# Optimization experiments

Measured on AMD Instinct MI355X. Metric: run time of the kernel, lower is better.

Reference implementation:

```python
import jax, jax.numpy as jnp
import numpy as np

# SDNet-CTRL cfg constants
MU = 0.1          # FISTA step size (cfg['MODEL']['MU'])
LMBD = 0.1        # sparsity weight (cfg['MODEL']['LAMBDA'][0])
N_STEPS = 4       # FISTA iterations (cfg['MODEL']['NUM_LAYERS'])
EPS_BN = 1e-5


def _conv(x, w, stride, padding):
    # torch F.conv2d, NCHW / OIHW
    return jax.lax.conv_general_dilated(
        x, w, window_strides=(stride, stride),
        padding=[(padding, padding), (padding, padding)],
        dimension_numbers=('NCHW', 'OIHW', 'NCHW'))


def _conv_t(c, w, stride, padding):
    # torch F.conv_transpose2d(c, w, stride, padding) with output_padding chosen
    # so that it exactly inverts the spatial map of _conv (k=4,s=2,p=1 -> 0).
    k = w.shape[2]
    w_t = jnp.flip(w, (2, 3)).transpose(1, 0, 2, 3)  # (I,O,k,k) flipped
    pad = k - 1 - padding
    return jax.lax.conv_general_dilated(
        c, w_t, window_strides=(1, 1),
        padding=[(pad, pad), (pad, pad)],
        lhs_dilation=(stride, stride),
        dimension_numbers=('NCHW', 'OIHW', 'NCHW'))


def _shrink_nn(c, thr):
    # non-negative soft threshold (cfg NONEGATIVE=True)
    return jax.nn.relu(c - thr)


def _dict_conv(x, w, stride, padding):
    # DictBlock: FISTA convolutional sparse coding, n_dict=1, w_norm=True.
    # normalize each dictionary atom (output filter) to unit l2 norm
    wn = w * jax.lax.rsqrt(jnp.sum(w * w, axis=(1, 2, 3), keepdims=True))
    ss = MU
    thr = LMBD * ss
    # t = 0
    c = _shrink_nn(ss * _conv(x, wn, stride, padding), thr)
    c_pre_pre = jnp.zeros_like(c)
    c_pre = c
    tk = 1.0
    for t in range(1, N_STEPS):
        tk_pre = tk
        tk = (1.0 + float(np.sqrt(1.0 + 4.0 * tk_pre * tk_pre))) / 2.0
        y = c_pre + ((tk_pre - 1.0) / tk) * (c_pre - c_pre_pre)
        r = x - _conv_t(y, wn, stride, padding)      # residual in image space
        c = _shrink_nn(y + ss * _conv(r, wn, stride, padding), thr)
        c_pre_pre, c_pre = c_pre, c
    return c


def _bn(x, g, b):
    # training-mode BatchNorm2d (batch statistics)
    m = jnp.mean(x, axis=(0, 2, 3), keepdims=True)
    v = jnp.var(x, axis=(0, 2, 3), keepdims=True)
    return g.reshape(1, -1, 1, 1) * (x - m) * jax.lax.rsqrt(v + EPS_BN) + b.reshape(1, -1, 1, 1)


def _lrelu(x):
    return jnp.where(x >= 0, x, 0.2 * x)


def setup_inputs() -> dict:
    key = jax.random.key(0)
    ks = jax.random.split(key, 5)
    nc, ndf, nz = 3, 128, 256
    B, H = 256, 32

    def mk_w(k, o, i):
        return jax.random.normal(k, (o, i, 4, 4), jnp.float32) * 0.02

    return {
        'x': jax.random.normal(ks[0], (B, nc, H, H), jnp.float32),
        'w1': mk_w(ks[1], ndf, nc),
        'w2': mk_w(ks[2], 2 * ndf, ndf),
        'w3': mk_w(ks[3], 4 * ndf, 2 * ndf),
        'w4': mk_w(ks[4], nz, 4 * ndf),
        'g2': jnp.ones((2 * ndf,), jnp.float32),
        'b2': jnp.zeros((2 * ndf,), jnp.float32),
        'g3': jnp.ones((4 * ndf,), jnp.float32),
        'b3': jnp.zeros((4 * ndf,), jnp.float32),
    }


def reference(x, w1, w2, w3, w4, g2, b2, g3, b3):
    h = _lrelu(_dict_conv(x, w1, 2, 1))                 # (B, ndf, 16, 16)
    h = _lrelu(_bn(_dict_conv(h, w2, 2, 1), g2, b2))    # (B, 2ndf, 8, 8)
    h = _lrelu(_bn(_dict_conv(h, w3, 2, 1), g3, b3))    # (B, 4ndf, 4, 4)
    h = _dict_conv(h, w4, 1, 0)                         # (B, nz, 1, 1)
    h = h.reshape(h.shape[0], -1)                       # Flatten
    n = jnp.sqrt(jnp.sum(h * h, axis=1, keepdims=True))
    return h / jnp.maximum(n, 1e-12)                    # F.normalize(dim=1)
```

## Files before the change

### kernel.cpp

```cpp
#include <hip/hip_runtime.h>
#include <math.h>

#define SS   0.1f
#define THRC 0.01f

typedef __attribute__((ext_vector_type(8))) short s16x8;
typedef __attribute__((ext_vector_type(4))) float f32x4;

__device__ __forceinline__ float b2f(unsigned short u){
  union{unsigned int i; float f;} v; v.i = ((unsigned int)u)<<16; return v.f;
}
__device__ __forceinline__ unsigned short f2b(float f){
  union{float f; unsigned int i;} v; v.f = f;
  return (unsigned short)((v.i + 0x7fffu + ((v.i>>16)&1u))>>16);
}
__device__ __forceinline__ s16x8 as_s16x8(uint4 u){
  union{uint4 a; s16x8 b;} c; c.a = u; return c.b;
}
__device__ __forceinline__ int swz8(int row, int q){ return (row<<3) | (q ^ (row&7)); }

__device__ __forceinline__ void gld16(const void* g, void* l){
  __builtin_amdgcn_global_load_lds(
      (const __attribute__((address_space(1))) unsigned int*)g,
      (__attribute__((address_space(3))) unsigned int*)l, 16, 0, 0);
}

enum { EPI_FIRST=0, EPI_UPDATE=1, EPI_PARTIAL=2, EPI_RES_NHWC=3, EPI_RES_FLAT=4 };

struct EpiM {
  unsigned short* C;
  const unsigned short* Y;
  const unsigned short* Cprev;
  unsigned short* Yout;
  const unsigned short* img;
  const unsigned short* zp;
  float coef;
  int lH, lW, lC;
  int S_MN, Kc;
};

struct LA_ident {
  const unsigned short* A; int K;
  __device__ void setz(int){}
  __device__ __forceinline__ const unsigned short* addr(int m, int k8) const {
    return A + (size_t)m*K + ((size_t)k8<<3);
  }
};
struct LA_nhwc {
  const unsigned short* img; const unsigned short* zp; int lH, lW, lC;
  __device__ void setz(int){}
  __device__ __forceinline__ const unsigned short* addr(int m, int k8) const {
    int lWo = lW-1, lHo = lH-1;
    int wo = m & ((1<<lWo)-1); int t = m>>lWo; int ho = t & ((1<<lHo)-1); int b = t>>lHo;
    int k = k8<<3; int kk = k>>lC; int i = k & ((1<<lC)-1);
    int kw = kk&3, kh = kk>>2;
    int h = 2*ho + kh - 1, w = 2*wo + kw - 1;
    if ((unsigned)h >= (1u<<lH) || (unsigned)w >= (1u<<lW)) return zp;
    return img + (((((((size_t)b<<lH)|h)<<lW)|w))<<lC) + i;
  }
};
struct LA_yg {
  const unsigned short* y; const unsigned short* zp; int lHo, lWo, lO, ph, pw;
  __device__ void setz(int z){ ph = z>>1; pw = z&1; }
  __device__ __forceinline__ const unsigned short* addr(int m, int k8) const {
    int l = m & ((1<<lWo)-1); int t = m>>lWo; int j = t & ((1<<lHo)-1); int b = t>>lHo;
    int k = k8<<3; int tt = k>>lO; int o = k & ((1<<lO)-1);
    int th = tt>>1, tw = tt&1;
    int ho = ph ? (j+1-th) : (j-th);
    int wo = pw ? (l+1-tw) : (l-tw);
    if ((unsigned)ho >= (1u<<lHo) || (unsigned)wo >= (1u<<lWo)) return zp;
    return y + (((((((size_t)b<<lHo)|ho)<<lWo)|wo))<<lO) + o;
  }
};
struct LA_padb {
  const unsigned short* img;
  __device__ void setz(int){}
  __device__ __forceinline__ const unsigned short* addr(int m, int k8) const {
    int wo = m&15, t = m>>4, ho = t&15, b = t>>4;
    int kh = k8>>1, kw0 = (k8&1)<<1;
    int h = 2*ho + kh, w = 2*wo + kw0;
    return img + (((size_t)b*34 + h)*34 + w)*4;
  }
};

template<class AL, int EPI>
__global__ __launch_bounds__(512)
void mgemm_k(AL al, const unsigned short* __restrict__ Bw, int M, int N, int K, EpiM ep)
{
  __shared__ uint4 S[2][2048];
  const int tid = threadIdx.x;
  const int bm = blockIdx.y<<7, bn = blockIdx.x<<7;
  const int z = blockIdx.z;
  int kb = 0, ke = K;
  const unsigned short* Bp = Bw;
  if (EPI == EPI_PARTIAL){ kb = z*ep.Kc; ke = kb + ep.Kc; }
  if (EPI == EPI_RES_NHWC){ Bp = Bw + (size_t)z*(size_t)N*K; al.setz(z); }

  f32x4 acc[4][2];
  #pragma unroll
  for (int i=0;i<4;++i)
    #pragma unroll
    for (int j=0;j<2;++j){ acc[i][j][0]=0.f; acc[i][j][1]=0.f; acc[i][j][2]=0.f; acc[i][j][3]=0.f; }

  const int lane = tid & 63, wid = tid >> 6;
  const int wm = (wid>>2)<<6, wn = (wid&3)<<5;
  const int fr = lane & 15, fq = lane >> 4;

  auto issue = [&](int k0, int b){
    int k8 = k0>>3;
    #pragma unroll
    for (int i=0;i<2;++i){
      int s  = (wid<<7) + (i<<6) + lane;
      int sr = s>>3, q = (s&7) ^ (sr&7);
      gld16(al.addr(bm+sr, k8+q), (void*)&S[b][(wid<<7) + (i<<6)]);
    }
    #pragma unroll
    for (int i=0;i<2;++i){
      int s  = (wid<<7) + (i<<6) + lane;
      int sr = s>>3, q = (s&7) ^ (sr&7);
      int gn = bn + sr;
      const unsigned short* src = (gn < N) ? Bp + (size_t)gn*K + ((size_t)(k8+q)<<3) : ep.zp;
      gld16(src, (void*)&S[b][1024 + (wid<<7) + (i<<6)]);
    }
  };

  issue(kb, 0);
  int buf = 0;
  for (int k0 = kb; k0 < ke; k0 += 64){
    asm volatile("s_waitcnt vmcnt(0)" ::: "memory");
    __builtin_amdgcn_s_barrier();
    __builtin_amdgcn_sched_barrier(0);
    if (k0 + 64 < ke) issue(k0 + 64, buf^1);
    const uint4* As = &S[buf][0];
    const uint4* Bs = &S[buf][1024];
    #pragma unroll
    for (int half=0; half<2; ++half){
      const int qb = (half<<2) | fq;
      s16x8 af[4], bf[2];
      #pragma unroll
      for (int mi=0;mi<4;++mi) af[mi] = as_s16x8(As[swz8(wm + mi*16 + fr, qb)]);
      #pragma unroll
      for (int ni=0;ni<2;++ni) bf[ni] = as_s16x8(Bs[swz8(wn + ni*16 + fr, qb)]);
      #pragma unroll
      for (int mi=0;mi<4;++mi)
        #pragma unroll
        for (int ni=0;ni<2;++ni)
          acc[mi][ni] = __builtin_amdgcn_mfma_f32_16x16x32_bf16(af[mi], bf[ni], acc[mi][ni], 0,0,0);
    }
    buf ^= 1;
  }

  #pragma unroll
  for (int mi=0;mi<4;++mi){
    #pragma unroll
    for (int ni=0;ni<2;++ni){
      int n = bn + wn + ni*16 + fr;
      if (n >= N) continue;
      int mb = bm + wm + mi*16 + (fq<<2);
      #pragma unroll
      for (int r=0;r<4;++r){
        int m = mb + r;
        float a = acc[mi][ni][r];
        if (EPI == EPI_FIRST){
          float v = SS*a - THRC; v = v>0.f ? v : 0.f;
          ep.C[(size_t)m*N + n] = f2b(v);
        } else if (EPI == EPI_UPDATE){
          size_t idx = (size_t)m*N + n;
          float v = b2f(ep.Y[idx]) + SS*a - THRC; v = v>0.f ? v : 0.f;
          ep.C[idx] = f2b(v);
          if (ep.Yout) ep.Yout[idx] = f2b(v + ep.coef*(v - b2f(ep.Cprev[idx])));
        } else if (EPI == EPI_PARTIAL){
          ep.C[(size_t)z*ep.S_MN + (size_t)m*N + n] = f2b(a);
        } else if (EPI == EPI_RES_NHWC){
          int lWo = ep.lW-1, lHo = ep.lH-1;
          int l = m & ((1<<lWo)-1); int t = m>>lWo; int j = t & ((1<<lHo)-1); int b = t>>lHo;
          int h = 2*j + (z>>1), w = 2*l + (z&1);
          size_t ridx = (((((((size_t)b<<ep.lH)|h)<<ep.lW)|w))<<ep.lC) | n;
          ep.C[ridx] = f2b(b2f(ep.img[ridx]) - a);
        } else {
          size_t ridx = (size_t)m*N + n;
          ep.C[ridx] = f2b(b2f(ep.img[ridx]) - a);
        }
      }
    }
  }
}

__global__ __launch_bounds__(64)
void wnorm1_k(const float* __restrict__ w, unsigned short* __restrict__ wf1,
              unsigned short* __restrict__ wcolT)
{
  int o = blockIdx.x, tid = threadIdx.x;
  __shared__ float red[64];
  float v = (tid < 48) ? w[(size_t)o*48 + tid] : 0.f;
  red[tid] = v*v; __syncthreads();
  for (int d=32; d>0; d>>=1){ if (tid<d) red[tid] += red[tid+d]; __syncthreads(); }
  float nv = v * rsqrtf(red[0]);
  if (tid < 48){
    int c = tid>>4, t = tid&15;
    wf1[(size_t)o*64 + t*4 + c] = f2b(nv);
    wcolT[(size_t)(t*4+c)*128 + o] = f2b(nv);
  } else {
    int t = tid - 48;
    wf1[(size_t)o*64 + t*4 + 3] = 0;
    wcolT[(size_t)(t*4+3)*128 + o] = 0;
  }
}
__global__ __launch_bounds__(256)
void wnormX_k(const float* __restrict__ w, int Cin, int O,
              unsigned short* __restrict__ wT, unsigned short* __restrict__ wclsT,
              unsigned short* __restrict__ wEO)
{
  int o = blockIdx.x, tid = threadIdx.x; int E = Cin*16;
  __shared__ float red[256];
  float s = 0.f;
  for (int e = tid; e < E; e += 256){ float v = w[(size_t)o*E + e]; s += v*v; }
  red[tid] = s; __syncthreads();
  for (int d=128; d>0; d>>=1){ if (tid<d) red[tid] += red[tid+d]; __syncthreads(); }
  float scale = rsqrtf(red[0]);
  for (int e = tid; e < E; e += 256){
    float v = w[(size_t)o*E + e] * scale;
    int i = e>>4, t = e&15, kh = t>>2, kw = t&3;
    int ee = t*Cin + i;
    if (wT)  wT[(size_t)o*E + ee] = f2b(v);
    if (wEO) wEO[(size_t)ee*O + o] = f2b(v);
    if (wclsT){
      int ph = (kh&1)^1, pw = (kw&1)^1, cls = ph*2+pw;
      int tt = (kh>>1)*2 + (kw>>1);
      wclsT[(((size_t)cls*Cin + i)*4 + tt)*O + o] = f2b(v);
    }
  }
}

__global__ void splitk_shrink_k(const unsigned short* __restrict__ part,
                                const unsigned short* __restrict__ Y,
                                unsigned short* __restrict__ C,
                                unsigned short* __restrict__ Yout,
                                const unsigned short* __restrict__ Cprev,
                                float coef, int MN, int S)
{
  for (int i = blockIdx.x*blockDim.x + threadIdx.x; i < MN; i += gridDim.x*blockDim.x){
    float s = 0.f;
    for (int zz = 0; zz < S; ++zz) s += b2f(part[(size_t)zz*MN + i]);
    float v = (Y ? b2f(Y[i]) : 0.f) + SS*s - THRC; v = v>0.f ? v : 0.f;
    C[i] = f2b(v);
    if (Yout) Yout[i] = f2b(v + coef*(v - b2f(Cprev[i])));
  }
}

__global__ void pad_x_k(const float* __restrict__ x, unsigned short* __restrict__ xpb){
  int idx = blockIdx.x*256 + threadIdx.x;
  if (idx >= 262144) return;
  int w = idx&31, t = idx>>5, h = t&31, b = t>>5;
  size_t src = (size_t)b*3072 + h*32 + w;
  unsigned short* d = xpb + (((size_t)b*34 + h+1)*34 + w+1)*4;
  d[0] = f2b(x[src]); d[1] = f2b(x[src+1024]); d[2] = f2b(x[src+2048]); d[3] = 0;
}

__global__ void l1_resid_k(const unsigned short* __restrict__ Col,
                           const float* __restrict__ x, unsigned short* __restrict__ r1pb)
{
  int idx = blockIdx.x*256 + threadIdx.x;
  if (idx >= 262144) return;
  int w = idx&31, t = idx>>5, h = t&31, b = t>>5;
  float a0=0.f, a1=0.f, a2=0.f;
  #pragma unroll
  for (int kh=0; kh<4; ++kh){
    int hh = h+1-kh; if (hh & 1) continue; int ho = hh>>1; if ((unsigned)ho >= 16u) continue;
    #pragma unroll
    for (int kw=0; kw<4; ++kw){
      int ww = w+1-kw; if (ww & 1) continue; int wo = ww>>1; if ((unsigned)wo >= 16u) continue;
      int m = (b*16+ho)*16+wo;
      const unsigned short* cp = Col + (size_t)m*64 + (kh*4+kw)*4;
      a0 += b2f(cp[0]); a1 += b2f(cp[1]); a2 += b2f(cp[2]);
    }
  }
  size_t src = (size_t)b*3072 + h*32 + w;
  unsigned short* d = r1pb + (((size_t)b*34 + h+1)*34 + w+1)*4;
  d[0] = f2b(x[src] - a0); d[1] = f2b(x[src+1024] - a1); d[2] = f2b(x[src+2048] - a2); d[3] = 0;
}

__global__ void bn_stats_k(const unsigned short* __restrict__ d, float* __restrict__ sums,
                           int rows, int O){
  for (int c = threadIdx.x; c < O; c += blockDim.x){
    float a = 0.f, b = 0.f;
    for (int r = blockIdx.x; r < rows; r += gridDim.x){
      float v = b2f(d[(size_t)r*O + c]); a += v; b += v*v;
    }
    atomicAdd(&sums[c], a); atomicAdd(&sums[O+c], b);
  }
}
__global__ void bn_apply_k(const unsigned short* __restrict__ d, const float* __restrict__ sums,
                           const float* __restrict__ g, const float* __restrict__ bta,
                           unsigned short* __restrict__ outp, int rows, int O, float inv_cnt){
  int total = rows*O;
  for (int i = blockIdx.x*blockDim.x + threadIdx.x; i < total; i += gridDim.x*blockDim.x){
    int c = i % O;
    float mean = sums[c]*inv_cnt;
    float var  = sums[O+c]*inv_cnt - mean*mean;
    float v = g[c]*(b2f(d[i])-mean)*rsqrtf(var + 1e-5f) + bta[c];
    outp[i] = f2b(v >= 0.f ? v : 0.2f*v);
  }
}

__global__ __launch_bounds__(256)
void norm_rows_k(const unsigned short* __restrict__ h, float* __restrict__ out){
  int row = blockIdx.x, tid = threadIdx.x;
  __shared__ float red[256];
  float v = b2f(h[(size_t)row*256 + tid]);
  red[tid] = v*v; __syncthreads();
  for (int d=128; d>0; d>>=1){ if (tid<d) red[tid] += red[tid+d]; __syncthreads(); }
  float nrm = sqrtf(red[0]); nrm = nrm > 1e-12f ? nrm : 1e-12f;
  out[(size_t)row*256 + tid] = v / nrm;
}

extern "C" void kernel_launch(void* const* d_in, const int* in_sizes, int n_in,
                              void* d_out, int out_size, void* d_ws, size_t ws_size,
                              hipStream_t stream)
{
  const float* x  = (const float*)d_in[0];
  const float* w1 = (const float*)d_in[1];
  const float* w2 = (const float*)d_in[2];
  const float* w3 = (const float*)d_in[3];
  const float* w4 = (const float*)d_in[4];
  const float* g2 = (const float*)d_in[5];
  const float* b2 = (const float*)d_in[6];
  const float* g3 = (const float*)d_in[7];
  const float* b3 = (const float*)d_in[8];
  float* out = (float*)d_out;

  char* p = (char*)d_ws;
  auto ah = [&](size_t n){ unsigned short* r = (unsigned short*)p; p += n*2; return r; };
  auto af = [&](size_t n){ float* r = (float*)p; p += n*4; return r; };

  unsigned short* wf1    = ah(128*64);
  unsigned short* wcol1T = ah(64*128);
  unsigned short* wT2    = ah((size_t)256*2048);
  unsigned short* wcls2  = ah((size_t)4*128*1024);
  unsigned short* wT3    = ah((size_t)512*4096);
  unsigned short* wcls3  = ah((size_t)4*256*2048);
  unsigned short* wT4    = ah((size_t)256*8192);
  unsigned short* wE4    = ah((size_t)8192*256);
  unsigned short* h1     = ah((size_t)8388608);
  unsigned short* h2     = ah((size_t)4194304);
  unsigned short* h3     = ah((size_t)2097152);
  unsigned short* cA     = ah((size_t)8388608);
  unsigned short* cB     = ah((size_t)8388608);
  unsigned short* yA     = ah((size_t)8388608);
  unsigned short* yB     = ah((size_t)8388608);
  unsigned short* rH     = ah((size_t)8388608);
  char* regionA = p; p += 17858560;
  unsigned short* Col    = (unsigned short*)regionA;
  unsigned short* xpb    = (unsigned short*)(regionA + 8388608);
  unsigned short* r1pb   = (unsigned short*)(regionA + 8388608 + 2367488);
  unsigned short* partL3 = (unsigned short*)regionA;
  unsigned short* partL4 = (unsigned short*)regionA;
  float* bnsum = af(1024);
  unsigned short* zp16 = ah(128);

  double tk = 1.0; float coef[4] = {0.f,0.f,0.f,0.f};
  for (int t = 1; t < 4; ++t){
    double tkp = tk; tk = (1.0 + sqrt(1.0 + 4.0*tkp*tkp))*0.5;
    coef[t] = (float)((tkp - 1.0)/tk);
  }

  hipMemsetAsync(zp16, 0, 256, stream);
  hipMemsetAsync(xpb,  0, 2367488, stream);
  hipMemsetAsync(r1pb, 0, 2367488, stream);
  pad_x_k<<<1024,256,0,stream>>>(x, xpb);
  wnorm1_k<<<128, 64, 0, stream>>>(w1, wf1, wcol1T);
  wnormX_k<<<256,256,0,stream>>>(w2, 128, 256, wT2, wcls2, nullptr);
  wnormX_k<<<512,256,0,stream>>>(w3, 256, 512, wT3, wcls3, nullptr);
  wnormX_k<<<256,256,0,stream>>>(w4, 512, 256, wT4, nullptr, wE4);

  auto l1_fwd = [&](const unsigned short* src, const unsigned short* Y, const unsigned short* Cp,
                    unsigned short* Cout, unsigned short* Yout, float cf){
    LA_padb al{src};
    EpiM ep{}; ep.C=Cout; ep.Y=Y; ep.Cprev=Cp; ep.Yout=Yout; ep.coef=cf; ep.zp=zp16;
    dim3 g(1, 512, 1);
    if (Y) mgemm_k<LA_padb,EPI_UPDATE><<<g,512,0,stream>>>(al, wf1, 65536,128,64, ep);
    else   mgemm_k<LA_padb,EPI_FIRST ><<<g,512,0,stream>>>(al, wf1, 65536,128,64, ep);
  };
  auto l1_tconv = [&](const unsigned short* y){
    LA_ident al{y, 128};
    EpiM ep{}; ep.C=Col; ep.S_MN=0; ep.Kc=128; ep.zp=zp16;
    mgemm_k<LA_ident,EPI_PARTIAL><<<dim3(1,512,1),512,0,stream>>>(al, wcol1T, 65536,64,128, ep);
    l1_resid_k<<<1024,256,0,stream>>>(Col, x, r1pb);
  };
  l1_fwd(xpb,  nullptr, nullptr, cA, nullptr, 0.f);
  l1_tconv(cA);
  l1_fwd(r1pb, cA, cA, cB, yA, coef[2]);
  l1_tconv(yA);
  l1_fwd(r1pb, yA, cB, cA, yB, coef[3]);
  l1_tconv(yB);
  l1_fwd(r1pb, yB, nullptr, h1, nullptr, 0.f);

  auto l2_fwd = [&](const unsigned short* src, const unsigned short* Y, const unsigned short* Cp,
                    unsigned short* Cout, unsigned short* Yout, float cf){
    LA_nhwc al{src, zp16, 4,4,7};
    EpiM ep{}; ep.C=Cout; ep.Y=Y; ep.Cprev=Cp; ep.Yout=Yout; ep.coef=cf; ep.zp=zp16;
    dim3 g(2, 128, 1);
    if (Y) mgemm_k<LA_nhwc,EPI_UPDATE><<<g,512,0,stream>>>(al, wT2, 16384,256,2048, ep);
    else   mgemm_k<LA_nhwc,EPI_FIRST ><<<g,512,0,stream>>>(al, wT2, 16384,256,2048, ep);
  };
  auto l2_tconv = [&](const unsigned short* y){
    LA_yg al{y, zp16, 3,3,8, 0,0};
    EpiM ep{}; ep.C=rH; ep.img=h1; ep.lH=4; ep.lW=4; ep.lC=7; ep.zp=zp16;
    mgemm_k<LA_yg,EPI_RES_NHWC><<<dim3(1,128,4),512,0,stream>>>(al, wcls2, 16384,128,1024, ep);
  };
  l2_fwd(h1, nullptr, nullptr, cA, nullptr, 0.f);
  l2_tconv(cA);
  l2_fwd(rH, cA, cA, cB, yA, coef[2]);
  l2_tconv(yA);
  l2_fwd(rH, yA, cB, cA, yB, coef[3]);
  l2_tconv(yB);
  l2_fwd(rH, yB, nullptr, cB, nullptr, 0.f);
  hipMemsetAsync(bnsum, 0, 2*256*sizeof(float), stream);
  bn_stats_k<<<256,256,0,stream>>>(cB, bnsum, 16384, 256);
  bn_apply_k<<<2048,256,0,stream>>>(cB, bnsum, g2, b2, h2, 16384, 256, 1.f/16384.f);

  auto l3_fwd = [&](const unsigned short* src, const unsigned short* Y, const unsigned short* Cp,
                    unsigned short* Cout, unsigned short* Yout, float cf){
    LA_nhwc al{src, zp16, 3,3,8};
    EpiM ep{}; ep.C=partL3; ep.S_MN=4096*512; ep.Kc=1024; ep.zp=zp16;
    mgemm_k<LA_nhwc,EPI_PARTIAL><<<dim3(4,32,4),512,0,stream>>>(al, wT3, 4096,512,4096, ep);
    splitk_shrink_k<<<1024,256,0,stream>>>(partL3, Y, Cout, Yout, Cp, cf, 4096*512, 4);
  };
  auto l3_tconv = [&](const unsigned short* y){
    LA_yg al{y, zp16, 2,2,9, 0,0};
    EpiM ep{}; ep.C=rH; ep.img=h2; ep.lH=3; ep.lW=3; ep.lC=8; ep.zp=zp16;
    mgemm_k<LA_yg,EPI_RES_NHWC><<<dim3(2,32,4),512,0,stream>>>(al, wcls3, 4096,256,2048, ep);
  };
  l3_fwd(h2, nullptr, nullptr, cA, nullptr, 0.f);
  l3_tconv(cA);
  l3_fwd(rH, cA, cA, cB, yA, coef[2]);
  l3_tconv(yA);
  l3_fwd(rH, yA, cB, cA, yB, coef[3]);
  l3_tconv(yB);
  l3_fwd(rH, yB, nullptr, cB, nullptr, 0.f);
  hipMemsetAsync(bnsum, 0, 2*512*sizeof(float), stream);
  bn_stats_k<<<256,256,0,stream>>>(cB, bnsum, 4096, 512);
  bn_apply_k<<<2048,256,0,stream>>>(cB, bnsum, g3, b3, h3, 4096, 512, 1.f/4096.f);

  auto l4_fwd = [&](const unsigned short* Asrc, const unsigned short* Y, const unsigned short* Cp,
                    unsigned short* Cout, unsigned short* Yout, float cf){
    LA_ident al{Asrc, 8192};
    EpiM ep{}; ep.C=partL4; ep.S_MN=65536; ep.Kc=256; ep.zp=zp16;
    mgemm_k<LA_ident,EPI_PARTIAL><<<dim3(2,2,32),512,0,stream>>>(al, wT4, 256,256,8192, ep);
    splitk_shrink_k<<<256,256,0,stream>>>(partL4, Y, Cout, Yout, Cp, cf, 65536, 32);
  };
  auto l4_tconv = [&](const unsigned short* y){
    LA_ident al{y, 256};
    EpiM ep{}; ep.C=rH; ep.img=h3; ep.zp=zp16;
    mgemm_k<LA_ident,EPI_RES_FLAT><<<dim3(64,2,1),512,0,stream>>>(al, wE4, 256,8192,256, ep);
  };
  l4_fwd(h3, nullptr, nullptr, cA, nullptr, 0.f);
  l4_tconv(cA);
  l4_fwd(rH, cA, cA, cB, yA, coef[2]);
  l4_tconv(yA);
  l4_fwd(rH, yA, cB, cA, yB, coef[3]);
  l4_tconv(yB);
  l4_fwd(rH, yB, nullptr, cB, nullptr, 0.f);

  norm_rows_k<<<256,256,0,stream>>>(cB, out);
}
```

Before: 889.3 us.

## Load GEMM B operand straight into registers, using 256-thread blocks

The shared GEMM kernel now runs with 256 threads and four waves instead of eight. Each wave computes a 64x64 sub-tile with a 4x4 grid of accumulators. Only the A tile is staged through LDS; the B fragments are read directly from global memory into registers, which are double-buffered across a k-loop unrolled by two. This halves LDS use and the number of barriers per tile, and should allow two blocks per CU. The cost is more accumulator registers and B reads that are not shared between waves. Those reads are scattered 16-byte loads and lose the old zero-pointer bounds guard when N is smaller than the tile width.

```diff
diff --git a/kernel.cpp b/kernel.cpp
--- a/kernel.cpp
+++ b/kernel.cpp
@@ -84,10 +84,10 @@
 };
 
 template<class AL, int EPI>
-__global__ __launch_bounds__(512)
+__global__ __launch_bounds__(256, 2)
 void mgemm_k(AL al, const unsigned short* __restrict__ Bw, int M, int N, int K, EpiM ep)
 {
-  __shared__ uint4 S[2][2048];
+  __shared__ uint4 S[2][1024];
   const int tid = threadIdx.x;
   const int bm = blockIdx.y<<7, bn = blockIdx.x<<7;
   const int z = blockIdx.z;
@@ -96,64 +96,70 @@
   if (EPI == EPI_PARTIAL){ kb = z*ep.Kc; ke = kb + ep.Kc; }
   if (EPI == EPI_RES_NHWC){ Bp = Bw + (size_t)z*(size_t)N*K; al.setz(z); }
 
-  f32x4 acc[4][2];
+  f32x4 acc[4][4];
   #pragma unroll
   for (int i=0;i<4;++i)
     #pragma unroll
-    for (int j=0;j<2;++j){ acc[i][j][0]=0.f; acc[i][j][1]=0.f; acc[i][j][2]=0.f; acc[i][j][3]=0.f; }
+    for (int j=0;j<4;++j){ acc[i][j][0]=0.f; acc[i][j][1]=0.f; acc[i][j][2]=0.f; acc[i][j][3]=0.f; }
 
   const int lane = tid & 63, wid = tid >> 6;
-  const int wm = (wid>>2)<<6, wn = (wid&3)<<5;
+  const int wm = (wid>>1)<<6, wn = (wid&1)<<6;
   const int fr = lane & 15, fq = lane >> 4;
 
-  auto issue = [&](int k0, int b){
+  auto issueA = [&](int k0, int b){
     int k8 = k0>>3;
     #pragma unroll
-    for (int i=0;i<2;++i){
-      int s  = (wid<<7) + (i<<6) + lane;
+    for (int i=0;i<4;++i){
+      int s  = (wid<<8) + (i<<6) + lane;
       int sr = s>>3, q = (s&7) ^ (sr&7);
-      gld16(al.addr(bm+sr, k8+q), (void*)&S[b][(wid<<7) + (i<<6)]);
-    }
-    #pragma unroll
-    for (int i=0;i<2;++i){
-      int s  = (wid<<7) + (i<<6) + lane;
-      int sr = s>>3, q = (s&7) ^ (sr&7);
-      int gn = bn + sr;
-      const unsigned short* src = (gn < N) ? Bp + (size_t)gn*K + ((size_t)(k8+q)<<3) : ep.zp;
-      gld16(src, (void*)&S[b][1024 + (wid<<7) + (i<<6)]);
-    }
-  };
-
-  issue(kb, 0);
+      gld16(al.addr(bm+sr, k8+q), (void*)&S[b][(wid<<8) + (i<<6)]);
+    }
+  };
+  auto loadB = [&](int k0, int ni, int half)->uint4{
+    int n = bn + wn + ni*16 + fr;
+    return *(const uint4*)(Bp + (size_t)n*K + k0 + (((half<<2)|fq)<<3));
+  };
+
+  uint4 bA[8], bB[8];
+  issueA(kb, 0);
+  #pragma unroll
+  for (int ni=0;ni<4;++ni){ bA[ni*2+0]=loadB(kb,ni,0); bA[ni*2+1]=loadB(kb,ni,1); }
+
   int buf = 0;
-  for (int k0 = kb; k0 < ke; k0 += 64){
+  auto stepf = [&](int k0, uint4 (&cur)[8], uint4 (&nxt)[8]){
     asm volatile("s_waitcnt vmcnt(0)" ::: "memory");
     __builtin_amdgcn_s_barrier();
     __builtin_amdgcn_sched_barrier(0);
-    if (k0 + 64 < ke) issue(k0 + 64, buf^1);
+    if (k0 + 64 < ke){
+      issueA(k0 + 64, buf^1);
+      #pragma unroll
+      for (int ni=0;ni<4;++ni){ nxt[ni*2+0]=loadB(k0+64,ni,0); nxt[ni*2+1]=loadB(k0+64,ni,1); }
+    }
     const uint4* As = &S[buf][0];
-    const uint4* Bs = &S[buf][1024];
     #pragma unroll
     for (int half=0; half<2; ++half){
       const int qb = (half<<2) | fq;
-      s16x8 af[4], bf[2];
+      s16x8 af[4];
       #pragma unroll
       for (int mi=0;mi<4;++mi) af[mi] = as_s16x8(As[swz8(wm + mi*16 + fr, qb)]);
       #pragma unroll
-      for (int ni=0;ni<2;++ni) bf[ni] = as_s16x8(Bs[swz8(wn + ni*16 + fr, qb)]);
-      #pragma unroll
       for (int mi=0;mi<4;++mi)
         #pragma unroll
-        for (int ni=0;ni<2;++ni)
-          acc[mi][ni] = __builtin_amdgcn_mfma_f32_16x16x32_bf16(af[mi], bf[ni], acc[mi][ni], 0,0,0);
+        for (int ni=0;ni<4;++ni)
+          acc[mi][ni] = __builtin_amdgcn_mfma_f32_16x16x32_bf16(
+              af[mi], as_s16x8(cur[ni*2+half]), acc[mi][ni], 0,0,0);
     }
     buf ^= 1;
+  };
+  for (int k0 = kb; k0 < ke; k0 += 128){
+    stepf(k0, bA, bB);
+    if (k0 + 64 < ke) stepf(k0+64, bB, bA);
   }
 
   #pragma unroll
   for (int mi=0;mi<4;++mi){
     #pragma unroll
-    for (int ni=0;ni<2;++ni){
+    for (int ni=0;ni<4;++ni){
       int n = bn + wn + ni*16 + fr;
       if (n >= N) continue;
       int mb = bm + wm + mi*16 + (fq<<2);
@@ -378,13 +384,13 @@
     LA_padb al{src};
     EpiM ep{}; ep.C=Cout; ep.Y=Y; ep.Cprev=Cp; ep.Yout=Yout; ep.coef=cf; ep.zp=zp16;
     dim3 g(1, 512, 1);
-    if (Y) mgemm_k<LA_padb,EPI_UPDATE><<<g,512,0,stream>>>(al, wf1, 65536,128,64, ep);
-    else   mgemm_k<LA_padb,EPI_FIRST ><<<g,512,0,stream>>>(al, wf1, 65536,128,64, ep);
+    if (Y) mgemm_k<LA_padb,EPI_UPDATE><<<g,256,0,stream>>>(al, wf1, 65536,128,64, ep);
+    else   mgemm_k<LA_padb,EPI_FIRST ><<<g,256,0,stream>>>(al, wf1, 65536,128,64, ep);
   };
   auto l1_tconv = [&](const unsigned short* y){
     LA_ident al{y, 128};
     EpiM ep{}; ep.C=Col; ep.S_MN=0; ep.Kc=128; ep.zp=zp16;
-    mgemm_k<LA_ident,EPI_PARTIAL><<<dim3(1,512,1),512,0,stream>>>(al, wcol1T, 65536,64,128, ep);
+    mgemm_k<LA_ident,EPI_PARTIAL><<<dim3(1,512,1),256,0,stream>>>(al, wcol1T, 65536,64,128, ep);
     l1_resid_k<<<1024,256,0,stream>>>(Col, x, r1pb);
   };
   l1_fwd(xpb,  nullptr, nullptr, cA, nullptr, 0.f);
@@ -400,13 +406,13 @@
     LA_nhwc al{src, zp16, 4,4,7};
     EpiM ep{}; ep.C=Cout; ep.Y=Y; ep.Cprev=Cp; ep.Yout=Yout; ep.coef=cf; ep.zp=zp16;
     dim3 g(2, 128, 1);
-    if (Y) mgemm_k<LA_nhwc,EPI_UPDATE><<<g,512,0,stream>>>(al, wT2, 16384,256,2048, ep);
-    else   mgemm_k<LA_nhwc,EPI_FIRST ><<<g,512,0,stream>>>(al, wT2, 16384,256,2048, ep);
+    if (Y) mgemm_k<LA_nhwc,EPI_UPDATE><<<g,256,0,stream>>>(al, wT2, 16384,256,2048, ep);
+    else   mgemm_k<LA_nhwc,EPI_FIRST ><<<g,256,0,stream>>>(al, wT2, 16384,256,2048, ep);
   };
   auto l2_tconv = [&](const unsigned short* y){
     LA_yg al{y, zp16, 3,3,8, 0,0};
     EpiM ep{}; ep.C=rH; ep.img=h1; ep.lH=4; ep.lW=4; ep.lC=7; ep.zp=zp16;
-    mgemm_k<LA_yg,EPI_RES_NHWC><<<dim3(1,128,4),512,0,stream>>>(al, wcls2, 16384,128,1024, ep);
+    mgemm_k<LA_yg,EPI_RES_NHWC><<<dim3(1,128,4),256,0,stream>>>(al, wcls2, 16384,128,1024, ep);
   };
   l2_fwd(h1, nullptr, nullptr, cA, nullptr, 0.f);
   l2_tconv(cA);
@@ -423,13 +429,13 @@
                     unsigned short* Cout, unsigned short* Yout, float cf){
     LA_nhwc al{src, zp16, 3,3,8};
     EpiM ep{}; ep.C=partL3; ep.S_MN=4096*512; ep.Kc=1024; ep.zp=zp16;
-    mgemm_k<LA_nhwc,EPI_PARTIAL><<<dim3(4,32,4),512,0,stream>>>(al, wT3, 4096,512,4096, ep);
+    mgemm_k<LA_nhwc,EPI_PARTIAL><<<dim3(4,32,4),256,0,stream>>>(al, wT3, 4096,512,4096, ep);
     splitk_shrink_k<<<1024,256,0,stream>>>(partL3, Y, Cout, Yout, Cp, cf, 4096*512, 4);
   };
   auto l3_tconv = [&](const unsigned short* y){
     LA_yg al{y, zp16, 2,2,9, 0,0};
     EpiM ep{}; ep.C=rH; ep.img=h2; ep.lH=3; ep.lW=3; ep.lC=8; ep.zp=zp16;
-    mgemm_k<LA_yg,EPI_RES_NHWC><<<dim3(2,32,4),512,0,stream>>>(al, wcls3, 4096,256,2048, ep);
+    mgemm_k<LA_yg,EPI_RES_NHWC><<<dim3(2,32,4),256,0,stream>>>(al, wcls3, 4096,256,2048, ep);
   };
   l3_fwd(h2, nullptr, nullptr, cA, nullptr, 0.f);
   l3_tconv(cA);
@@ -446,13 +452,13 @@
                     unsigned short* Cout, unsigned short* Yout, float cf){
     LA_ident al{Asrc, 8192};
     EpiM ep{}; ep.C=partL4; ep.S_MN=65536; ep.Kc=256; ep.zp=zp16;
-    mgemm_k<LA_ident,EPI_PARTIAL><<<dim3(2,2,32),512,0,stream>>>(al, wT4, 256,256,8192, ep);
+    mgemm_k<LA_ident,EPI_PARTIAL><<<dim3(2,2,32),256,0,stream>>>(al, wT4, 256,256,8192, ep);
     splitk_shrink_k<<<256,256,0,stream>>>(partL4, Y, Cout, Yout, Cp, cf, 65536, 32);
   };
   auto l4_tconv = [&](const unsigned short* y){
     LA_ident al{y, 256};
     EpiM ep{}; ep.C=rH; ep.img=h3; ep.zp=zp16;
-    mgemm_k<LA_ident,EPI_RES_FLAT><<<dim3(64,2,1),512,0,stream>>>(al, wE4, 256,8192,256, ep);
+    mgemm_k<LA_ident,EPI_RES_FLAT><<<dim3(64,2,1),256,0,stream>>>(al, wE4, 256,8192,256, ep);
   };
   l4_fwd(h3, nullptr, nullptr, cA, nullptr, 0.f);
   l4_tconv(cA);
```

New measurement: 1.366 ms. +53.6%, slower.

## Triple-buffer LDS in bf16 GEMM and interleave fragment loads with MFMA

Applied to the files above, without the earlier changes.

The main MFMA GEMM kernel moves from double to triple buffering in LDS, prefetching two K-tiles ahead with split A/B global->LDS issues and partial vmcnt waits. LDS fragment reads for the next half-tile are software-pipelined against MFMAs of the current half, and s_setprio raises priority around the MFMA bursts. The goal is to hide global load latency and LDS read latency behind matrix math. In exchange it uses 1.5x the LDS per block, which may lower occupancy, and adds an extra barrier per iteration.

```diff
diff --git a/kernel.cpp b/kernel.cpp
--- a/kernel.cpp
+++ b/kernel.cpp
@@ -87,7 +87,7 @@
 __global__ __launch_bounds__(512)
 void mgemm_k(AL al, const unsigned short* __restrict__ Bw, int M, int N, int K, EpiM ep)
 {
-  __shared__ uint4 S[2][2048];
+  __shared__ uint4 S[3][2048];
   const int tid = threadIdx.x;
   const int bm = blockIdx.y<<7, bn = blockIdx.x<<7;
   const int z = blockIdx.z;
@@ -106,7 +106,7 @@
   const int wm = (wid>>2)<<6, wn = (wid&3)<<5;
   const int fr = lane & 15, fq = lane >> 4;
 
-  auto issue = [&](int k0, int b){
+  auto issueA = [&](int k0, int b){
     int k8 = k0>>3;
     #pragma unroll
     for (int i=0;i<2;++i){
@@ -114,6 +114,9 @@
       int sr = s>>3, q = (s&7) ^ (sr&7);
       gld16(al.addr(bm+sr, k8+q), (void*)&S[b][(wid<<7) + (i<<6)]);
     }
+  };
+  auto issueB = [&](int k0, int b){
+    int k8 = k0>>3;
     #pragma unroll
     for (int i=0;i<2;++i){
       int s  = (wid<<7) + (i<<6) + lane;
@@ -124,30 +127,73 @@
     }
   };
 
-  issue(kb, 0);
-  int buf = 0;
-  for (int k0 = kb; k0 < ke; k0 += 64){
+  const int NT = (ke - kb) >> 6;
+  issueA(kb, 0); issueB(kb, 0);
+  if (NT > 1){
+    issueA(kb+64, 1); issueB(kb+64, 1);
+    asm volatile("s_waitcnt vmcnt(4)" ::: "memory");
+  } else {
     asm volatile("s_waitcnt vmcnt(0)" ::: "memory");
+  }
+  __builtin_amdgcn_s_barrier();
+  __builtin_amdgcn_sched_barrier(0);
+
+  s16x8 a0[4], b0[2], a1[4], b1[2];
+  {
+    const uint4* As = &S[0][0]; const uint4* Bs = &S[0][1024];
+    #pragma unroll
+    for (int mi=0;mi<4;++mi) a0[mi] = as_s16x8(As[swz8(wm + mi*16 + fr, fq)]);
+    #pragma unroll
+    for (int ni=0;ni<2;++ni) b0[ni] = as_s16x8(Bs[swz8(wn + ni*16 + fr, fq)]);
+  }
+  __builtin_amdgcn_sched_barrier(0);
+
+  int t = 0;
+  for (int k0 = kb; k0 < ke; k0 += 64, ++t){
+    const int bufc = t%3, bufn = (t+1)%3, buf2 = (t+2)%3;
+    {
+      const uint4* As = &S[bufc][0]; const uint4* Bs = &S[bufc][1024];
+      #pragma unroll
+      for (int mi=0;mi<4;++mi) a1[mi] = as_s16x8(As[swz8(wm + mi*16 + fr, 4|fq)]);
+      #pragma unroll
+      for (int ni=0;ni<2;++ni) b1[ni] = as_s16x8(Bs[swz8(wn + ni*16 + fr, 4|fq)]);
+    }
+    __builtin_amdgcn_sched_barrier(0);
+    if (k0 + 128 < ke) issueA(k0 + 128, buf2);
+    __builtin_amdgcn_s_setprio(1);
+    #pragma unroll
+    for (int mi=0;mi<4;++mi)
+      #pragma unroll
+      for (int ni=0;ni<2;++ni)
+        acc[mi][ni] = __builtin_amdgcn_mfma_f32_16x16x32_bf16(a0[mi], b0[ni], acc[mi][ni], 0,0,0);
+    __builtin_amdgcn_s_setprio(0);
+    __builtin_amdgcn_sched_barrier(0);
+    if (k0 + 128 < ke) issueB(k0 + 128, buf2);
+    if (k0 + 64 < ke){
+      if (k0 + 128 < ke) asm volatile("s_waitcnt vmcnt(4)" ::: "memory");
+      else               asm volatile("s_waitcnt vmcnt(0)" ::: "memory");
+    }
     __builtin_amdgcn_s_barrier();
     __builtin_amdgcn_sched_barrier(0);
-    if (k0 + 64 < ke) issue(k0 + 64, buf^1);
-    const uint4* As = &S[buf][0];
-    const uint4* Bs = &S[buf][1024];
-    #pragma unroll
-    for (int half=0; half<2; ++half){
-      const int qb = (half<<2) | fq;
-      s16x8 af[4], bf[2];
-      #pragma unroll
-      for (int mi=0;mi<4;++mi) af[mi] = as_s16x8(As[swz8(wm + mi*16 + fr, qb)]);
-      #pragma unroll
-      for (int ni=0;ni<2;++ni) bf[ni] = as_s16x8(Bs[swz8(wn + ni*16 + fr, qb)]);
-      #pragma unroll
-      for (int mi=0;mi<4;++mi)
-        #pragma unroll
-        for (int ni=0;ni<2;++ni)
-          acc[mi][ni] = __builtin_amdgcn_mfma_f32_16x16x32_bf16(af[mi], bf[ni], acc[mi][ni], 0,0,0);
-    }
-    buf ^= 1;
+    if (k0 + 64 < ke){
+      const uint4* As = &S[bufn][0]; const uint4* Bs = &S[bufn][1024];
+      #pragma unroll
+      for (int mi=0;mi<4;++mi) a0[mi] = as_s16x8(As[swz8(wm + mi*16 + fr, fq)]);
+      #pragma unroll
+      for (int ni=0;ni<2;++ni) b0[ni] = as_s16x8(Bs[swz8(wn + ni*16 + fr, fq)]);
+    }
+    __builtin_amdgcn_sched_barrier(0);
+    __builtin_amdgcn_s_setprio(1);
+    #pragma unroll
+    for (int mi=0;mi<4;++mi)
+      #pragma unroll
+      for (int ni=0;ni<2;++ni)
+        acc[mi][ni] = __builtin_amdgcn_mfma_f32_16x16x32_bf16(a1[mi], b1[ni], acc[mi][ni], 0,0,0);
+    __builtin_amdgcn_s_setprio(0);
+    if (k0 + 64 < ke){
+      __builtin_amdgcn_s_barrier();
+      __builtin_amdgcn_sched_barrier(0);
+    }
   }
 
   #pragma unroll
@@ -173,7 +219,7 @@
           ep.C[(size_t)z*ep.S_MN + (size_t)m*N + n] = f2b(a);
         } else if (EPI == EPI_RES_NHWC){
           int lWo = ep.lW-1, lHo = ep.lH-1;
-          int l = m & ((1<<lWo)-1); int t = m>>lWo; int j = t & ((1<<lHo)-1); int b = t>>lHo;
+          int l = m & ((1<<lWo)-1); int t2 = m>>lWo; int j = t2 & ((1<<lHo)-1); int b = t2>>lHo;
           int h = 2*j + (z>>1), w = 2*l + (z&1);
           size_t ridx = (((((((size_t)b<<ep.lH)|h)<<ep.lW)|w))<<ep.lC) | n;
           ep.C[ridx] = f2b(b2f(ep.img[ridx]) - a);
```

New measurement: 1.027 ms. 15.5% more time.

## Stage GEMM tiles through registers and add BK=128 K-tile template

Applied to the files above, without the earlier changes.

Replaces the direct global-to-LDS async loads with register-staged prefetch: the next tile is loaded into registers while the current one is consumed from LDS, then written to the alternate LDS buffer. Adds a template K-tile size (64 or 128) with matching swizzle, and uses BK=128 for most GEMMs to halve barrier count per K. Costs more VGPRs and doubles LDS per block, which may reduce occupancy.

```diff
diff --git a/kernel.cpp b/kernel.cpp
--- a/kernel.cpp
+++ b/kernel.cpp
@@ -16,13 +16,6 @@
 }
 __device__ __forceinline__ s16x8 as_s16x8(uint4 u){
   union{uint4 a; s16x8 b;} c; c.a = u; return c.b;
-}
-__device__ __forceinline__ int swz8(int row, int q){ return (row<<3) | (q ^ (row&7)); }
-
-__device__ __forceinline__ void gld16(const void* g, void* l){
-  __builtin_amdgcn_global_load_lds(
-      (const __attribute__((address_space(1))) unsigned int*)g,
-      (__attribute__((address_space(3))) unsigned int*)l, 16, 0, 0);
 }
 
 enum { EPI_FIRST=0, EPI_UPDATE=1, EPI_PARTIAL=2, EPI_RES_NHWC=3, EPI_RES_FLAT=4 };
@@ -83,11 +76,17 @@
   }
 };
 
-template<class AL, int EPI>
+template<class AL, int EPI, int BK>
 __global__ __launch_bounds__(512)
 void mgemm_k(AL al, const unsigned short* __restrict__ Bw, int M, int N, int K, EpiM ep)
 {
-  __shared__ uint4 S[2][2048];
+  constexpr int QR    = BK/8;
+  constexpr int QM    = QR-1;
+  constexpr int QS    = (BK==128)?4:3;
+  constexpr int SLOTS = 128*QR;
+  constexpr int NI    = QR/4;
+  __shared__ uint4 As[2*SLOTS];
+  __shared__ uint4 Bs[2*SLOTS];
   const int tid = threadIdx.x;
   const int bm = blockIdx.y<<7, bn = blockIdx.x<<7;
   const int z = blockIdx.z;
@@ -106,41 +105,48 @@
   const int wm = (wid>>2)<<6, wn = (wid&3)<<5;
   const int fr = lane & 15, fq = lane >> 4;
 
-  auto issue = [&](int k0, int b){
+  uint4 ra[NI], rb[NI];
+  auto fetch = [&](int k0){
     int k8 = k0>>3;
     #pragma unroll
-    for (int i=0;i<2;++i){
-      int s  = (wid<<7) + (i<<6) + lane;
-      int sr = s>>3, q = (s&7) ^ (sr&7);
-      gld16(al.addr(bm+sr, k8+q), (void*)&S[b][(wid<<7) + (i<<6)]);
-    }
-    #pragma unroll
-    for (int i=0;i<2;++i){
-      int s  = (wid<<7) + (i<<6) + lane;
-      int sr = s>>3, q = (s&7) ^ (sr&7);
+    for (int i=0;i<NI;++i){
+      int s  = wid*(NI*64) + (i<<6) + lane;
+      int sr = s>>QS, q = (s&QM) ^ (sr&QM);
+      ra[i] = *(const uint4*)al.addr(bm+sr, k8+q);
       int gn = bn + sr;
-      const unsigned short* src = (gn < N) ? Bp + (size_t)gn*K + ((size_t)(k8+q)<<3) : ep.zp;
-      gld16(src, (void*)&S[b][1024 + (wid<<7) + (i<<6)]);
-    }
-  };
-
-  issue(kb, 0);
+      rb[i] = (gn < N) ? *(const uint4*)(Bp + (size_t)gn*K + k0 + (q<<3))
+                       : *(const uint4*)ep.zp;
+    }
+  };
+
+  fetch(kb);
   int buf = 0;
-  for (int k0 = kb; k0 < ke; k0 += 64){
-    asm volatile("s_waitcnt vmcnt(0)" ::: "memory");
+  for (int k0 = kb; k0 < ke; k0 += BK){
+    const int base = buf*SLOTS;
+    #pragma unroll
+    for (int i=0;i<NI;++i){
+      int s = wid*(NI*64) + (i<<6) + lane;
+      As[base + s] = ra[i];
+      Bs[base + s] = rb[i];
+    }
+    if (k0 + BK < ke) fetch(k0 + BK);
+    asm volatile("s_waitcnt lgkmcnt(0)" ::: "memory");
     __builtin_amdgcn_s_barrier();
     __builtin_amdgcn_sched_barrier(0);
-    if (k0 + 64 < ke) issue(k0 + 64, buf^1);
-    const uint4* As = &S[buf][0];
-    const uint4* Bs = &S[buf][1024];
-    #pragma unroll
-    for (int half=0; half<2; ++half){
-      const int qb = (half<<2) | fq;
+    #pragma unroll
+    for (int c=0; c<BK/32; ++c){
+      const int qb = (c<<2) | fq;
       s16x8 af[4], bf[2];
       #pragma unroll
-      for (int mi=0;mi<4;++mi) af[mi] = as_s16x8(As[swz8(wm + mi*16 + fr, qb)]);
+      for (int mi=0;mi<4;++mi){
+        int row = wm + mi*16 + fr;
+        af[mi] = as_s16x8(As[base + (row<<QS) + (qb ^ (row&QM))]);
+      }
       #pragma unroll
-      for (int ni=0;ni<2;++ni) bf[ni] = as_s16x8(Bs[swz8(wn + ni*16 + fr, qb)]);
+      for (int ni=0;ni<2;++ni){
+        int row = wn + ni*16 + fr;
+        bf[ni] = as_s16x8(Bs[base + (row<<QS) + (qb ^ (row&QM))]);
+      }
       #pragma unroll
       for (int mi=0;mi<4;++mi)
         #pragma unroll
@@ -173,7 +179,7 @@
           ep.C[(size_t)z*ep.S_MN + (size_t)m*N + n] = f2b(a);
         } else if (EPI == EPI_RES_NHWC){
           int lWo = ep.lW-1, lHo = ep.lH-1;
-          int l = m & ((1<<lWo)-1); int t = m>>lWo; int j = t & ((1<<lHo)-1); int b = t>>lHo;
+          int l = m & ((1<<lWo)-1); int t2 = m>>lWo; int j = t2 & ((1<<lHo)-1); int b = t2>>lHo;
           int h = 2*j + (z>>1), w = 2*l + (z&1);
           size_t ridx = (((((((size_t)b<<ep.lH)|h)<<ep.lW)|w))<<ep.lC) | n;
           ep.C[ridx] = f2b(b2f(ep.img[ridx]) - a);
@@ -378,13 +384,13 @@
     LA_padb al{src};
     EpiM ep{}; ep.C=Cout; ep.Y=Y; ep.Cprev=Cp; ep.Yout=Yout; ep.coef=cf; ep.zp=zp16;
     dim3 g(1, 512, 1);
-    if (Y) mgemm_k<LA_padb,EPI_UPDATE><<<g,512,0,stream>>>(al, wf1, 65536,128,64, ep);
-    else   mgemm_k<LA_padb,EPI_FIRST ><<<g,512,0,stream>>>(al, wf1, 65536,128,64, ep);
+    if (Y) mgemm_k<LA_padb,EPI_UPDATE,64><<<g,512,0,stream>>>(al, wf1, 65536,128,64, ep);
+    else   mgemm_k<LA_padb,EPI_FIRST ,64><<<g,512,0,stream>>>(al, wf1, 65536,128,64, ep);
   };
   auto l1_tconv = [&](const unsigned short* y){
     LA_ident al{y, 128};
     EpiM ep{}; ep.C=Col; ep.S_MN=0; ep.Kc=128; ep.zp=zp16;
-    mgemm_k<LA_ident,EPI_PARTIAL><<<dim3(1,512,1),512,0,stream>>>(al, wcol1T, 65536,64,128, ep);
+    mgemm_k<LA_ident,EPI_PARTIAL,128><<<dim3(1,512,1),512,0,stream>>>(al, wcol1T, 65536,64,128, ep);
     l1_resid_k<<<1024,256,0,stream>>>(Col, x, r1pb);
   };
   l1_fwd(xpb,  nullptr, nullptr, cA, nullptr, 0.f);
@@ -400,13 +406,13 @@
     LA_nhwc al{src, zp16, 4,4,7};
     EpiM ep{}; ep.C=Cout; ep.Y=Y; ep.Cprev=Cp; ep.Yout=Yout; ep.coef=cf; ep.zp=zp16;
     dim3 g(2, 128, 1);
-    if (Y) mgemm_k<LA_nhwc,EPI_UPDATE><<<g,512,0,stream>>>(al, wT2, 16384,256,2048, ep);
-    else   mgemm_k<LA_nhwc,EPI_FIRST ><<<g,512,0,stream>>>(al, wT2, 16384,256,2048, ep);
+    if (Y) mgemm_k<LA_nhwc,EPI_UPDATE,128><<<g,512,0,stream>>>(al, wT2, 16384,256,2048, ep);
+    else   mgemm_k<LA_nhwc,EPI_FIRST ,128><<<g,512,0,stream>>>(al, wT2, 16384,256,2048, ep);
   };
   auto l2_tconv = [&](const unsigned short* y){
     LA_yg al{y, zp16, 3,3,8, 0,0};
     EpiM ep{}; ep.C=rH; ep.img=h1; ep.lH=4; ep.lW=4; ep.lC=7; ep.zp=zp16;
-    mgemm_k<LA_yg,EPI_RES_NHWC><<<dim3(1,128,4),512,0,stream>>>(al, wcls2, 16384,128,1024, ep);
+    mgemm_k<LA_yg,EPI_RES_NHWC,128><<<dim3(1,128,4),512,0,stream>>>(al, wcls2, 16384,128,1024, ep);
   };
   l2_fwd(h1, nullptr, nullptr, cA, nullptr, 0.f);
   l2_tconv(cA);
@@ -423,13 +429,13 @@
                     unsigned short* Cout, unsigned short* Yout, float cf){
     LA_nhwc al{src, zp16, 3,3,8};
     EpiM ep{}; ep.C=partL3; ep.S_MN=4096*512; ep.Kc=1024; ep.zp=zp16;
-    mgemm_k<LA_nhwc,EPI_PARTIAL><<<dim3(4,32,4),512,0,stream>>>(al, wT3, 4096,512,4096, ep);
+    mgemm_k<LA_nhwc,EPI_PARTIAL,128><<<dim3(4,32,4),512,0,stream>>>(al, wT3, 4096,512,4096, ep);
     splitk_shrink_k<<<1024,256,0,stream>>>(partL3, Y, Cout, Yout, Cp, cf, 4096*512, 4);
   };
   auto l3_tconv = [&](const unsigned short* y){
     LA_yg al{y, zp16, 2,2,9, 0,0};
     EpiM ep{}; ep.C=rH; ep.img=h2; ep.lH=3; ep.lW=3; ep.lC=8; ep.zp=zp16;
-    mgemm_k<LA_yg,EPI_RES_NHWC><<<dim3(2,32,4),512,0,stream>>>(al, wcls3, 4096,256,2048, ep);
+    mgemm_k<LA_yg,EPI_RES_NHWC,128><<<dim3(2,32,4),512,0,stream>>>(al, wcls3, 4096,256,2048, ep);
   };
   l3_fwd(h2, nullptr, nullptr, cA, nullptr, 0.f);
   l3_tconv(cA);
@@ -446,13 +452,13 @@
                     unsigned short* Cout, unsigned short* Yout, float cf){
     LA_ident al{Asrc, 8192};
     EpiM ep{}; ep.C=partL4; ep.S_MN=65536; ep.Kc=256; ep.zp=zp16;
-    mgemm_k<LA_ident,EPI_PARTIAL><<<dim3(2,2,32),512,0,stream>>>(al, wT4, 256,256,8192, ep);
+    mgemm_k<LA_ident,EPI_PARTIAL,128><<<dim3(2,2,32),512,0,stream>>>(al, wT4, 256,256,8192, ep);
     splitk_shrink_k<<<256,256,0,stream>>>(partL4, Y, Cout, Yout, Cp, cf, 65536, 32);
   };
   auto l4_tconv = [&](const unsigned short* y){
     LA_ident al{y, 256};
     EpiM ep{}; ep.C=rH; ep.img=h3; ep.zp=zp16;
-    mgemm_k<LA_ident,EPI_RES_FLAT><<<dim3(64,2,1),512,0,stream>>>(al, wE4, 256,8192,256, ep);
+    mgemm_k<LA_ident,EPI_RES_FLAT,128><<<dim3(64,2,1),512,0,stream>>>(al, wE4, 256,8192,256, ep);
   };
   l4_fwd(h3, nullptr, nullptr, cA, nullptr, 0.f);
   l4_tconv(cA);
```

Result: slower. 1.955 ms (+119.8%).
